# Performance work log

Measured on AMD Instinct MI355X. Metric: run time of the kernel, lower is better.

## Reference

```python
import jax, jax.numpy as jnp
import numpy as np


def setup_inputs() -> dict:
    key = jax.random.key(0)
    k1, k2, k3 = jax.random.split(key, 3)
    B, T, F, U = 32, 4096, 512, 512
    x = jax.random.normal(k1, (B, T, F), dtype=jnp.float32)
    W = jax.random.normal(k2, (F, U), dtype=jnp.float32)
    b = jnp.zeros((U,), dtype=jnp.float32)
    V = jax.random.uniform(k3, (U, 1), dtype=jnp.float32)
    return {"x": x, "W": W, "b": b, "V": V}


def reference(x, W, b, V):
    # u = tanh(x @ W + b): [B, T, U]
    u = jnp.tanh(jnp.einsum('btf,fu->btu', x, W) + b)
    # scores = u @ V: [B, T, 1]; softmax over time (dim=1)
    a = jax.nn.softmax(jnp.einsum('btu,uo->bto', u, V), axis=1)
    # weighted sum pooling over time -> [B, F]
    return jnp.sum(x * a, axis=1)
```

## Files before the change

### kernel.cpp

```cpp
#include <hip/hip_runtime.h>


#define XT 4096
#define XF 512
#define XU 512

typedef __attribute__((ext_vector_type(8))) short short8;
typedef __attribute__((ext_vector_type(4))) short sh4;
typedef __attribute__((ext_vector_type(16))) float f32x16;

__device__ inline void cvt_hilo(float x, unsigned short &h, unsigned short &l) {
  unsigned u = __builtin_bit_cast(unsigned, x);
  h = (unsigned short)(u >> 16);
  float hf = __builtin_bit_cast(float, u & 0xFFFF0000u);
  float lo = x - hf;
  l = (unsigned short)(__builtin_bit_cast(unsigned, lo) >> 16);
}

__device__ inline float tanh_fast(float z) {
  float e = __expf(2.0f * z);
  return 1.0f - 2.0f * __builtin_amdgcn_rcpf(e + 1.0f);
}

__global__ void wconv_kernel(const float *__restrict__ W,
                             unsigned short *__restrict__ whi,
                             unsigned short *__restrict__ wlo) {
  int t2 = blockIdx.x * 256 + threadIdx.x;
  int l = t2 & 31;
  int g = (t2 >> 5) & 1;
  int t = (t2 >> 6) & 15;
  int s = t2 >> 10;
  short8 hv, lv;
#pragma unroll
  for (int j = 0; j < 8; ++j) {
    unsigned short h, lo;
    cvt_hilo(W[(size_t)(s * 16 + g * 8 + j) * XU + t * 32 + l], h, lo);
    hv[j] = (short)h;
    lv[j] = (short)lo;
  }
  size_t off = (size_t)s * 8192 + t * 512 + g * 256 + l * 8;
  *(short8 *)(whi + off) = hv;
  *(short8 *)(wlo + off) = lv;
}

#define MFMA(a, b, c) __builtin_amdgcn_mfma_f32_32x32x16_bf16(a, b, c, 0, 0, 0)

__global__ __launch_bounds__(512, 2)
void gemm_scores_kernel(const float *__restrict__ x,
                        const unsigned short *__restrict__ whi,
                        const unsigned short *__restrict__ wlo,
                        const float *__restrict__ bias,
                        const float *__restrict__ V,
                        float *__restrict__ partial,
                        float *__restrict__ pstats) {
  __shared__ unsigned short Abuf[2][4][2][512];
  __shared__ float scb[512];
  __shared__ float warr[128];
  __shared__ float red[1536];
  __shared__ float sarr[128];

  const int tid = threadIdx.x;
  const int lane = tid & 63;
  const int wave = tid >> 6;
  const int wr = wave >> 2;
  const int wc = wave & 3;
  const int l31 = lane & 31;
  const int half = lane >> 5;
  const size_t rowbase = (size_t)blockIdx.x * 128;

  f32x16 acc[2][4];
#pragma unroll
  for (int a = 0; a < 2; ++a)
#pragma unroll
    for (int c = 0; c < 4; ++c)
#pragma unroll
      for (int r = 0; r < 16; ++r) acc[a][c][r] = 0.f;

  const int srow = tid >> 2;
  const int sq = tid & 3;
  const float *sx = x + (rowbase + srow) * XF + sq * 4;
  const int widx = (sq >> 1) * 256 + (srow & 31) * 8 + (sq & 1) * 4;
  unsigned short *wb0 = &Abuf[0][srow >> 5][0][widx];
  unsigned short *wb1 = &Abuf[1][srow >> 5][0][widx];

  auto stage = [&](unsigned short *wb, float4 v) {
    sh4 h, l;
    unsigned short hh, ll;
    cvt_hilo(v.x, hh, ll); h[0] = (short)hh; l[0] = (short)ll;
    cvt_hilo(v.y, hh, ll); h[1] = (short)hh; l[1] = (short)ll;
    cvt_hilo(v.z, hh, ll); h[2] = (short)hh; l[2] = (short)ll;
    cvt_hilo(v.w, hh, ll); h[3] = (short)hh; l[3] = (short)ll;
    *(sh4 *)wb = h;
    *(sh4 *)(wb + 512) = l;
  };

  const unsigned short *whp = whi + (size_t)(wc * 4) * 512 + lane * 8;
  const unsigned short *wlp = wlo + (size_t)(wc * 4) * 512 + lane * 8;

  float4 xv = *(const float4 *)(sx);
  stage(wb0, xv);
  float4 xa = *(const float4 *)(sx + 16);
  __syncthreads();

#pragma unroll 2
  for (int s = 0; s < 32; ++s) {
    const int cur = s & 1;
    const unsigned short *p = whp + (size_t)s * 8192;
    const unsigned short *q = wlp + (size_t)s * 8192;
    short8 bh[4], bl[4];
#pragma unroll
    for (int cf = 0; cf < 4; ++cf) {
      bh[cf] = *(const short8 *)(p + cf * 512);
      bl[cf] = *(const short8 *)(q + cf * 512);
    }
    const unsigned short *ab0 = &Abuf[cur][wr * 2 + 0][0][0] + lane * 8;
    const unsigned short *ab1 = &Abuf[cur][wr * 2 + 1][0][0] + lane * 8;
    short8 ah0 = *(const short8 *)(ab0);
    short8 al0 = *(const short8 *)(ab0 + 512);
    short8 ah1 = *(const short8 *)(ab1);
    short8 al1 = *(const short8 *)(ab1 + 512);

    float4 xb = xa;
    if (s < 30) xb = *(const float4 *)(sx + (s + 2) * 16);

#pragma unroll
    for (int cf = 0; cf < 4; ++cf) {
      acc[0][cf] = MFMA(ah0, bh[cf], acc[0][cf]);
      acc[1][cf] = MFMA(ah1, bh[cf], acc[1][cf]);
      acc[0][cf] = MFMA(al0, bh[cf], acc[0][cf]);
      acc[1][cf] = MFMA(al1, bh[cf], acc[1][cf]);
      acc[0][cf] = MFMA(ah0, bl[cf], acc[0][cf]);
      acc[1][cf] = MFMA(ah1, bl[cf], acc[1][cf]);
    }

    if (s < 31) stage(cur ? wb0 : wb1, xa);
    __syncthreads();
    xa = xb;
  }

  float sc[2][16];
#pragma unroll
  for (int rf = 0; rf < 2; ++rf)
#pragma unroll
    for (int r = 0; r < 16; ++r) sc[rf][r] = 0.f;

#pragma unroll
  for (int cf = 0; cf < 4; ++cf) {
    int n = wc * 128 + cf * 32 + l31;
    float vv = V[n];
    float bb = bias[n];
#pragma unroll
    for (int rf = 0; rf < 2; ++rf)
#pragma unroll
      for (int r = 0; r < 16; ++r)
        sc[rf][r] += tanh_fast(acc[rf][cf][r] + bb) * vv;
  }
#pragma unroll
  for (int m = 1; m <= 16; m <<= 1) {
#pragma unroll
    for (int rf = 0; rf < 2; ++rf)
#pragma unroll
      for (int r = 0; r < 16; ++r)
        sc[rf][r] += __shfl_xor(sc[rf][r], m, 64);
  }
  if (l31 == 0) {
#pragma unroll
    for (int rf = 0; rf < 2; ++rf)
#pragma unroll
      for (int r = 0; r < 16; ++r) {
        int row = wr * 64 + rf * 32 + (r & 3) + 8 * (r >> 2) + 4 * half;
        scb[wc * 128 + row] = sc[rf][r];
      }
  }
  __syncthreads();

  if (tid < 128)
    sarr[tid] = scb[tid] + scb[128 + tid] + scb[256 + tid] + scb[384 + tid];
  __syncthreads();
  float mloc = -1e30f;
#pragma unroll 8
  for (int i = 0; i < 128; ++i) mloc = fmaxf(mloc, sarr[i]);
  if (tid < 128) warr[tid] = __expf(sarr[tid] - mloc);
  __syncthreads();

  float lsum = 0.f;
  if (tid < 64) {
    lsum = warr[tid] + warr[tid + 64];
#pragma unroll
    for (int m = 1; m < 64; m <<= 1) lsum += __shfl_xor(lsum, m, 64);
  }

  const int rg = tid >> 7;
  const int c4 = tid & 127;
  const float *xp = x + rowbase * XF;
  float4 pa = {0.f, 0.f, 0.f, 0.f};
#pragma unroll 8
  for (int i = 0; i < 32; ++i) {
    int r = rg * 32 + i;
    float4 v = *(const float4 *)(xp + (size_t)r * XF + c4 * 4);
    float wv = warr[r];
    pa.x += wv * v.x;
    pa.y += wv * v.y;
    pa.z += wv * v.z;
    pa.w += wv * v.w;
  }
  if (rg > 0) {
    float *rp = red + (rg - 1) * 512 + c4 * 4;
    rp[0] = pa.x; rp[1] = pa.y; rp[2] = pa.z; rp[3] = pa.w;
  }
  __syncthreads();
  if (rg == 0) {
    const float *r0 = red + c4 * 4;
    float4 o;
    o.x = pa.x + r0[0] + r0[512] + r0[1024];
    o.y = pa.y + r0[1] + r0[513] + r0[1025];
    o.z = pa.z + r0[2] + r0[514] + r0[1026];
    o.w = pa.w + r0[3] + r0[515] + r0[1027];
    *(float4 *)(partial + (size_t)blockIdx.x * 512 + c4 * 4) = o;
  }
  if (tid == 0) {
    pstats[blockIdx.x * 2] = mloc;
    pstats[blockIdx.x * 2 + 1] = lsum;
  }
}

__global__ __launch_bounds__(512)
void combine_kernel(const float *__restrict__ partial,
                    const float *__restrict__ pstats,
                    float *__restrict__ out) {
  int b = blockIdx.x;
  int f = threadIdx.x;
  __shared__ float ml[32], ll[32];
  if (f < 32) {
    ml[f] = pstats[(b * 32 + f) * 2];
    ll[f] = pstats[(b * 32 + f) * 2 + 1];
  }
  __syncthreads();
  float M = -1e30f;
#pragma unroll
  for (int c = 0; c < 32; ++c) M = fmaxf(M, ml[c]);
  float L = 0.f;
#pragma unroll
  for (int c = 0; c < 32; ++c) L += __expf(ml[c] - M) * ll[c];
  float acc = 0.f;
#pragma unroll
  for (int c = 0; c < 32; ++c)
    acc += __expf(ml[c] - M) * partial[(size_t)(b * 32 + c) * 512 + f];
  out[b * XF + f] = acc / L;
}

extern "C" void kernel_launch(void *const *d_in, const int *in_sizes, int n_in,
                              void *d_out, int out_size, void *d_ws,
                              size_t ws_size, hipStream_t stream) {
  const float *x = (const float *)d_in[0];
  const float *W = (const float *)d_in[1];
  const float *bias = (const float *)d_in[2];
  const float *V = (const float *)d_in[3];
  float *out = (float *)d_out;

  unsigned short *whi = (unsigned short *)d_ws;
  unsigned short *wlo = whi + 262144;
  float *partial = (float *)((char *)d_ws + 1048576);
  float *pstats = (float *)((char *)d_ws + 1048576 + 2097152);

  wconv_kernel<<<128, 256, 0, stream>>>(W, whi, wlo);
  gemm_scores_kernel<<<1024, 512, 0, stream>>>(x, whi, wlo, bias, V, partial,
                                               pstats);
  combine_kernel<<<32, 512, 0, stream>>>(partial, pstats, out);
}
```

Measured before the change: 542.9 us.

## Restructure GEMM into 32-row sub-tiles with smaller accumulators for higher occupancy

The 128-row block is now processed as four sequential 32-row sub-tiles. Each wave owns 64 output columns with two accumulators instead of a 2x4 grid of eight, and the launch bound rises from 2 to 4 blocks per CU. Each k-step also moves to a 64-wide chunk with a reworked LDS layout. The aim is to cut register pressure so more waves can be resident and hide memory latency. The cost is that each wave re-reads every W fragment from global memory/L2 four times per block, which lowers per-wave data reuse and adds more syncthreads.

After: 565.6 us. +4.2%, slower.

```diff
diff --git a/kernel.cpp b/kernel.cpp
--- a/kernel.cpp
+++ b/kernel.cpp
@@ -45,7 +45,7 @@
 
 #define MFMA(a, b, c) __builtin_amdgcn_mfma_f32_32x32x16_bf16(a, b, c, 0, 0, 0)
 
-__global__ __launch_bounds__(512, 2)
+__global__ __launch_bounds__(512, 4)
 void gemm_scores_kernel(const float *__restrict__ x,
                         const unsigned short *__restrict__ whi,
                         const unsigned short *__restrict__ wlo,
@@ -53,130 +53,114 @@
                         const float *__restrict__ V,
                         float *__restrict__ partial,
                         float *__restrict__ pstats) {
-  __shared__ unsigned short Abuf[2][4][2][512];
-  __shared__ float scb[512];
+  __shared__ unsigned short Abuf[2][4096];
+  __shared__ float scb[256];
+  __shared__ float sarr[128];
   __shared__ float warr[128];
   __shared__ float red[1536];
-  __shared__ float sarr[128];
 
   const int tid = threadIdx.x;
   const int lane = tid & 63;
-  const int wave = tid >> 6;
-  const int wr = wave >> 2;
-  const int wc = wave & 3;
+  const int w = tid >> 6;
   const int l31 = lane & 31;
   const int half = lane >> 5;
   const size_t rowbase = (size_t)blockIdx.x * 128;
 
-  f32x16 acc[2][4];
-#pragma unroll
-  for (int a = 0; a < 2; ++a)
-#pragma unroll
-    for (int c = 0; c < 4; ++c)
-#pragma unroll
-      for (int r = 0; r < 16; ++r) acc[a][c][r] = 0.f;
-
-  const int srow = tid >> 2;
-  const int sq = tid & 3;
-  const float *sx = x + (rowbase + srow) * XF + sq * 4;
-  const int widx = (sq >> 1) * 256 + (srow & 31) * 8 + (sq & 1) * 4;
-  unsigned short *wb0 = &Abuf[0][srow >> 5][0][widx];
-  unsigned short *wb1 = &Abuf[1][srow >> 5][0][widx];
-
-  auto stage = [&](unsigned short *wb, float4 v) {
+  const int srow = tid >> 4;
+  const int q = tid & 15;
+  const int widx = (q >> 2) * 1024 + ((q >> 1) & 1) * 256 + srow * 8 + (q & 1) * 4;
+
+  auto stage = [&](unsigned short *ab, float4 v) {
     sh4 h, l;
     unsigned short hh, ll;
     cvt_hilo(v.x, hh, ll); h[0] = (short)hh; l[0] = (short)ll;
     cvt_hilo(v.y, hh, ll); h[1] = (short)hh; l[1] = (short)ll;
     cvt_hilo(v.z, hh, ll); h[2] = (short)hh; l[2] = (short)ll;
     cvt_hilo(v.w, hh, ll); h[3] = (short)hh; l[3] = (short)ll;
-    *(sh4 *)wb = h;
-    *(sh4 *)(wb + 512) = l;
+    *(sh4 *)(ab + widx) = h;
+    *(sh4 *)(ab + widx + 512) = l;
   };
 
-  const unsigned short *whp = whi + (size_t)(wc * 4) * 512 + lane * 8;
-  const unsigned short *wlp = wlo + (size_t)(wc * 4) * 512 + lane * 8;
-
-  float4 xv = *(const float4 *)(sx);
-  stage(wb0, xv);
-  float4 xa = *(const float4 *)(sx + 16);
-  __syncthreads();
+  const unsigned short *whp = whi + (size_t)(w * 2) * 512 + lane * 8;
+  const unsigned short *wlp = wlo + (size_t)(w * 2) * 512 + lane * 8;
+
+#pragma unroll 1
+  for (int sub = 0; sub < 4; ++sub) {
+    f32x16 acc[2];
+#pragma unroll
+    for (int c = 0; c < 2; ++c)
+#pragma unroll
+      for (int r = 0; r < 16; ++r) acc[c][r] = 0.f;
+
+    const float *sx = x + (rowbase + sub * 32 + srow) * XF + q * 4;
+
+    float4 xa = *(const float4 *)sx;
+    stage(&Abuf[0][0], xa);
+    __syncthreads();
+
+#pragma unroll 1
+    for (int it = 0; it < 8; ++it) {
+      float4 xn;
+      if (it < 7) xn = *(const float4 *)(sx + (it + 1) * 64);
+
+      const unsigned short *abase = &Abuf[it & 1][0];
+      const unsigned short *pw = whp + (size_t)it * 32768;
+      const unsigned short *pl = wlp + (size_t)it * 32768;
 
 #pragma unroll 2
-  for (int s = 0; s < 32; ++s) {
-    const int cur = s & 1;
-    const unsigned short *p = whp + (size_t)s * 8192;
-    const unsigned short *q = wlp + (size_t)s * 8192;
-    short8 bh[4], bl[4];
-#pragma unroll
-    for (int cf = 0; cf < 4; ++cf) {
-      bh[cf] = *(const short8 *)(p + cf * 512);
-      bl[cf] = *(const short8 *)(q + cf * 512);
-    }
-    const unsigned short *ab0 = &Abuf[cur][wr * 2 + 0][0][0] + lane * 8;
-    const unsigned short *ab1 = &Abuf[cur][wr * 2 + 1][0][0] + lane * 8;
-    short8 ah0 = *(const short8 *)(ab0);
-    short8 al0 = *(const short8 *)(ab0 + 512);
-    short8 ah1 = *(const short8 *)(ab1);
-    short8 al1 = *(const short8 *)(ab1 + 512);
-
-    float4 xb = xa;
-    if (s < 30) xb = *(const float4 *)(sx + (s + 2) * 16);
-
-#pragma unroll
-    for (int cf = 0; cf < 4; ++cf) {
-      acc[0][cf] = MFMA(ah0, bh[cf], acc[0][cf]);
-      acc[1][cf] = MFMA(ah1, bh[cf], acc[1][cf]);
-      acc[0][cf] = MFMA(al0, bh[cf], acc[0][cf]);
-      acc[1][cf] = MFMA(al1, bh[cf], acc[1][cf]);
-      acc[0][cf] = MFMA(ah0, bl[cf], acc[0][cf]);
-      acc[1][cf] = MFMA(ah1, bl[cf], acc[1][cf]);
-    }
-
-    if (s < 31) stage(cur ? wb0 : wb1, xa);
+      for (int s16 = 0; s16 < 4; ++s16) {
+        short8 bh0 = *(const short8 *)(pw + s16 * 8192);
+        short8 bh1 = *(const short8 *)(pw + s16 * 8192 + 512);
+        short8 bl0 = *(const short8 *)(pl + s16 * 8192);
+        short8 bl1 = *(const short8 *)(pl + s16 * 8192 + 512);
+        short8 ah = *(const short8 *)(abase + s16 * 1024 + lane * 8);
+        short8 al = *(const short8 *)(abase + s16 * 1024 + 512 + lane * 8);
+        acc[0] = MFMA(ah, bh0, acc[0]);
+        acc[1] = MFMA(ah, bh1, acc[1]);
+        acc[0] = MFMA(al, bh0, acc[0]);
+        acc[1] = MFMA(al, bh1, acc[1]);
+        acc[0] = MFMA(ah, bl0, acc[0]);
+        acc[1] = MFMA(ah, bl1, acc[1]);
+      }
+
+      if (it < 7) stage(&Abuf[(it + 1) & 1][0], xn);
+      __syncthreads();
+    }
+
+    float sc[16];
+#pragma unroll
+    for (int r = 0; r < 16; ++r) sc[r] = 0.f;
+#pragma unroll
+    for (int cf = 0; cf < 2; ++cf) {
+      int n = w * 64 + cf * 32 + l31;
+      float vv = V[n];
+      float bb = bias[n];
+#pragma unroll
+      for (int r = 0; r < 16; ++r)
+        sc[r] += tanh_fast(acc[cf][r] + bb) * vv;
+    }
+#pragma unroll
+    for (int m = 1; m <= 16; m <<= 1) {
+#pragma unroll
+      for (int r = 0; r < 16; ++r) sc[r] += __shfl_xor(sc[r], m, 64);
+    }
+    if (l31 == 0) {
+#pragma unroll
+      for (int r = 0; r < 16; ++r) {
+        int row = (r & 3) + 8 * (r >> 2) + 4 * half;
+        scb[w * 32 + row] = sc[r];
+      }
+    }
     __syncthreads();
-    xa = xb;
-  }
-
-  float sc[2][16];
-#pragma unroll
-  for (int rf = 0; rf < 2; ++rf)
-#pragma unroll
-    for (int r = 0; r < 16; ++r) sc[rf][r] = 0.f;
-
-#pragma unroll
-  for (int cf = 0; cf < 4; ++cf) {
-    int n = wc * 128 + cf * 32 + l31;
-    float vv = V[n];
-    float bb = bias[n];
-#pragma unroll
-    for (int rf = 0; rf < 2; ++rf)
-#pragma unroll
-      for (int r = 0; r < 16; ++r)
-        sc[rf][r] += tanh_fast(acc[rf][cf][r] + bb) * vv;
-  }
-#pragma unroll
-  for (int m = 1; m <= 16; m <<= 1) {
-#pragma unroll
-    for (int rf = 0; rf < 2; ++rf)
-#pragma unroll
-      for (int r = 0; r < 16; ++r)
-        sc[rf][r] += __shfl_xor(sc[rf][r], m, 64);
-  }
-  if (l31 == 0) {
-#pragma unroll
-    for (int rf = 0; rf < 2; ++rf)
-#pragma unroll
-      for (int r = 0; r < 16; ++r) {
-        int row = wr * 64 + rf * 32 + (r & 3) + 8 * (r >> 2) + 4 * half;
-        scb[wc * 128 + row] = sc[rf][r];
-      }
-  }
-  __syncthreads();
-
-  if (tid < 128)
-    sarr[tid] = scb[tid] + scb[128 + tid] + scb[256 + tid] + scb[384 + tid];
-  __syncthreads();
+    if (tid < 32) {
+      float s = 0.f;
+#pragma unroll
+      for (int ww = 0; ww < 8; ++ww) s += scb[ww * 32 + tid];
+      sarr[sub * 32 + tid] = s;
+    }
+    __syncthreads();
+  }
+
   float mloc = -1e30f;
 #pragma unroll 8
   for (int i = 0; i < 128; ++i) mloc = fmaxf(mloc, sarr[i]);
```
